# Optimization experiments

Measured on AMD Instinct MI355X. Metric: run time of the kernel, lower is better.

## Reference

```python
import jax, jax.numpy as jnp
import numpy as np

E, S, V_OBS, OBJ, H, L, V_COMM = 64, 64, 128, 16, 256, 32, 32
K = 2 * OBJ  # expected number of nonzero indices per step


def prelu(x, a):
    return jnp.where(x >= 0, x, a * x)


def setup_inputs() -> dict:
    key = jax.random.key(0)
    ks = jax.random.split(key, 32)
    # obs: multi-hot with exactly K ones per (episode, step)
    u = jax.random.uniform(ks[0], (E, S, V_OBS))
    idx = jnp.argsort(u, axis=-1)[..., :K]
    obs = jax.nn.one_hot(idx, V_OBS, dtype=jnp.float32).sum(-2)
    comm = jax.random.normal(ks[1], (E, S, L, V_COMM), jnp.float32)

    def w(k, shape):
        return (jax.random.normal(k, shape, jnp.float32) * 0.05)

    a = lambda: jnp.asarray(0.25, jnp.float32)  # PReLU init
    b = lambda n: jnp.full((n,), 0.01, jnp.float32)
    return dict(
        obs=obs, comm=comm,
        obs_emb=w(ks[2], (V_OBS, H)), obs_a_emb=a(),
        obs_W=w(ks[3], (K * H, H)), obs_b=b(H), obs_a=a(),
        comm_emb=w(ks[4], (V_COMM, H)), comm_a_emb=a(),
        cw1=w(ks[5], (H // 4, H, 1)), cb1=b(H // 4),
        cw3=w(ks[6], (H // 4, H, 3)), cb3=b(H // 4),
        cw5=w(ks[7], (H // 4, H, 5)), cb5=b(H // 4),
        cw7=w(ks[8], (H // 4, H, 7)), cb7=b(H // 4),
        bn_g=jnp.ones((H,), jnp.float32), bn_b=jnp.zeros((H,), jnp.float32), cnn_a=a(),
        Wx=w(ks[9], (3, H, H)), bx=jnp.full((3, H), 0.01, jnp.float32),
        Wh=w(ks[10], (3, H, H)), bh=jnp.full((3, H), 0.01, jnp.float32),
        lin_a1=a(), lin_W=w(ks[11], (H, H)), lin_b=b(H), lin_a2=a(),
    )


def reference(obs, comm, obs_emb, obs_a_emb, obs_W, obs_b, obs_a,
              comm_emb, comm_a_emb, cw1, cb1, cw3, cb3, cw5, cb5, cw7, cb7,
              bn_g, bn_b, cnn_a, Wx, bx, Wh, bh, lin_a1, lin_W, lin_b, lin_a2):
    Ep, St, _ = obs.shape
    # extract_and_concatenate: ascending indices of the K ones per (episode, step)
    idx = jnp.argsort(-obs, axis=-1)[..., :K]          # stable sort -> ascending nonzero idx
    oe = prelu(obs_emb[idx], obs_a_emb)                # [E,S,K,H]
    o = prelu(oe.reshape(Ep, St, K * H) @ obs_W + obs_b, obs_a)  # [E,S,H]

    # comm path (comm already at max_comm_len, pad_zeros is identity)
    tok = jnp.argmax(comm, axis=-1)                    # [E,S,L]
    ce = prelu(comm_emb[tok], comm_a_emb)              # [E,S,L,H]
    x = ce.reshape(Ep * St, L, H).transpose(0, 2, 1)   # [N,H,L]
    dn = ('NCH', 'OIH', 'NCH')
    conv = lambda w_, b_: jax.lax.conv_general_dilated(
        x, w_, (1,), 'SAME', dimension_numbers=dn) + b_[None, :, None]
    y = jnp.concatenate([conv(cw1, cb1), conv(cw3, cb3),
                         conv(cw5, cb5), conv(cw7, cb7)], axis=1)  # [N,H,L]
    # BatchNorm1d (training-mode batch statistics over N and L)
    m = y.mean(axis=(0, 2), keepdims=True)
    v = y.var(axis=(0, 2), keepdims=True)
    y = bn_g[None, :, None] * (y - m) / jnp.sqrt(v + 1e-5) + bn_b[None, :, None]
    y = prelu(y, cnn_a).transpose(0, 2, 1)             # [N,L,H]

    # MTRNN (time_constant=True -> new=1, old=0): GRU-like gated cell
    xproj = jnp.einsum('nlh,ghk->glnk', y, Wx) + bx[:, None, None, :]  # [3,L,N,H]
    h0 = jnp.zeros((Ep * St, H), y.dtype)

    def step(h, xs):
        xr, xz, xn = xs
        r = jax.nn.sigmoid(xr + h @ Wh[0] + bh[0])
        z = jax.nn.sigmoid(xz + h @ Wh[1] + bh[1])
        n = jnp.tanh(xn + r * (h @ Wh[2] + bh[2]))
        return n * (1 - z) + h * z, None

    hN, _ = jax.lax.scan(step, h0, (xproj[0], xproj[1], xproj[2]))  # last step == outputs[:,-1]
    c = hN.reshape(Ep, St, H)
    c = prelu(prelu(c, lin_a1) @ lin_W + lin_b, lin_a2)
    return jnp.concatenate([o, c], axis=-1)           # [E,S,2H]
```

## Files before the change

### kernel.cpp

```cpp
#include <hip/hip_runtime.h>
#include <hip/hip_bf16.h>

#define N_ 4096
#define VOBS 128
#define KOBS 32
#define H_ 256
#define L_ 32
#define VCOMM 32

typedef __attribute__((ext_vector_type(8))) short short8;
typedef __attribute__((ext_vector_type(4))) float floatx4;

__device__ __forceinline__ float prelu_f(float x, float a){ return x >= 0.f ? x : a*x; }
__device__ __forceinline__ ushort f2bf(float x){
  unsigned int u = __float_as_uint(x);
  u = (u + 0x7FFFu + ((u >> 16) & 1u)) >> 16;
  return (ushort)u;
}
__device__ __forceinline__ float bf2f(ushort x){
  unsigned int u = ((unsigned int)x) << 16;
  return __uint_as_float(u);
}

__device__ __forceinline__ void gl_lds16(const ushort* __restrict__ src, ushort* dst){
  __builtin_amdgcn_global_load_lds(
      (const __attribute__((address_space(1))) unsigned int*)src,
      (__attribute__((address_space(3))) unsigned int*)dst, 16, 0, 0);
}


__global__ __launch_bounds__(256) void k_idx(const float* __restrict__ obs, int* __restrict__ idx){
  const int n = blockIdx.x*4 + (threadIdx.x >> 6);
  const int lane = threadIdx.x & 63;
  float v0 = obs[(size_t)n*VOBS + lane];
  float v1 = obs[(size_t)n*VOBS + 64 + lane];
  unsigned long long m0 = __ballot(v0 > 0.5f);
  unsigned long long m1 = __ballot(v1 > 0.5f);
  unsigned long long lt = (1ull << lane) - 1ull;
  if (v0 > 0.5f){
    int pos = __popcll(m0 & lt);
    if (pos < KOBS) idx[n*KOBS + pos] = lane;
  }
  if (v1 > 0.5f){
    int pos = __popcll(m0) + __popcll(m1 & lt);
    if (pos < KOBS) idx[n*KOBS + pos] = 64 + lane;
  }
}

__global__ __launch_bounds__(256) void k_contrib(
    const float* __restrict__ obs_emb, const float* __restrict__ a_emb_p,
    const float* __restrict__ obs_W, float* __restrict__ contrib){
  const int k = blockIdx.x;
  const int vbase = blockIdx.y*16;
  const int tid = threadIdx.x;
  __shared__ float pe[16][H_];
  float a = a_emb_p[0];
  for (int i = tid; i < 16*H_; i += 256){
    int v = i >> 8, j = i & 255;
    pe[v][j] = prelu_f(obs_emb[(size_t)(vbase+v)*H_ + j], a);
  }
  __syncthreads();
  float acc[16];
  #pragma unroll
  for (int v = 0; v < 16; ++v) acc[v] = 0.f;
  for (int j = 0; j < H_; ++j){
    float w = obs_W[((size_t)(k*H_ + j))*H_ + tid];
    #pragma unroll
    for (int v = 0; v < 16; ++v) acc[v] += pe[v][j]*w;
  }
  for (int v = 0; v < 16; ++v)
    contrib[((size_t)((vbase+v)*KOBS + k))*H_ + tid] = acc[v];
}

__global__ __launch_bounds__(256) void k_obs_o(
    const int* __restrict__ idx, const float* __restrict__ contrib,
    const float* __restrict__ obs_b, const float* __restrict__ obs_a_p,
    float* __restrict__ out){
  const int n = blockIdx.x, tid = threadIdx.x;
  __shared__ int id[KOBS];
  if (tid < KOBS) id[tid] = idx[n*KOBS + tid];
  __syncthreads();
  float acc = obs_b[tid];
  #pragma unroll 8
  for (int k = 0; k < KOBS; ++k)
    acc += contrib[((size_t)(id[k]*KOBS + k))*H_ + tid];
  out[(size_t)n*512 + tid] = prelu_f(acc, obs_a_p[0]);
}


__global__ void k_tok(const float* __restrict__ comm, int* __restrict__ tok){
  int i = blockIdx.x*blockDim.x + threadIdx.x;
  if (i >= N_*L_) return;
  const float4* p = (const float4*)(comm + (size_t)i*VCOMM);
  float best = -1e30f; int bi = 0;
  #pragma unroll
  for (int j = 0; j < 8; ++j){
    float4 q = p[j];
    if (q.x > best){ best = q.x; bi = j*4+0; }
    if (q.y > best){ best = q.y; bi = j*4+1; }
    if (q.z > best){ best = q.z; bi = j*4+2; }
    if (q.w > best){ best = q.w; bi = j*4+3; }
  }
  tok[i] = bi;
}

__global__ void k_P(const float* __restrict__ comm_emb, const float* __restrict__ ca_p,
                    const float* __restrict__ cw1, const float* __restrict__ cw3,
                    const float* __restrict__ cw5, const float* __restrict__ cw7,
                    float* __restrict__ P){
  const int slot = blockIdx.x, v = blockIdx.y, c = threadIdx.x;
  int g, tap;
  if (slot == 0){ g=0; tap=0; }
  else if (slot < 4){ g=1; tap=slot-1; }
  else if (slot < 9){ g=2; tap=slot-4; }
  else { g=3; tap=slot-9; }
  const float* w; int ks;
  if (g==0){ w=cw1; ks=1; } else if (g==1){ w=cw3; ks=3; }
  else if (g==2){ w=cw5; ks=5; } else { w=cw7; ks=7; }
  float a = ca_p[0];
  float acc = 0.f;
  for (int h = 0; h < H_; ++h){
    float e = prelu_f(comm_emb[(size_t)v*H_ + h], a);
    acc += e * w[(size_t)(c*H_ + h)*ks + tap];
  }
  P[(size_t)(slot*VCOMM + v)*64 + c] = acc;
}

template<int KS, bool APPLY>
__device__ __forceinline__ void conv_work(
    const float* __restrict__ Ps, const int tk[16][L_], int wave, int lane,
    float bias, float scale, float shift, float ca,
    ushort* __restrict__ ynorm, int nbase, int g,
    float* s_out, float* q_out)
{
  constexpr int PAD = (KS-1)/2;
  float s = 0.f, sq = 0.f;
  for (int j = 0; j < 4; ++j){
    const int nn = wave*4 + j;
    int base[L_];
    #pragma unroll
    for (int l = 0; l < L_; ++l) base[l] = tk[nn][l]*64 + lane;
    #pragma unroll
    for (int l = 0; l < L_; ++l){
      float acc = bias;
      #pragma unroll
      for (int t = 0; t < KS; ++t){
        const int lp = l + t - PAD;
        if (lp >= 0 && lp < L_) acc += Ps[t*2048 + base[lp]];
      }
      if (APPLY){
        float y = prelu_f(fmaf(acc, scale, shift), ca);
        ynorm[((size_t)l*N_ + (nbase+nn))*H_ + g*64 + lane] = f2bf(y);
      } else {
        s += acc; sq += acc*acc;
      }
    }
  }
  *s_out = s; *q_out = sq;
}

__global__ __launch_bounds__(256) void k_conv_stats(
    const int* __restrict__ tok, const float* __restrict__ P,
    const float* __restrict__ cb1, const float* __restrict__ cb3,
    const float* __restrict__ cb5, const float* __restrict__ cb7,
    float* __restrict__ stats){
  const int g = blockIdx.y;
  const int nbase = blockIdx.x*16;
  const int tid = threadIdx.x, lane = tid & 63, wave = tid >> 6;
  const int ks = 2*g + 1, base = g*g;
  const float* cb = (g==0)?cb1:(g==1)?cb3:(g==2)?cb5:cb7;
  const float bias = cb[lane];
  __shared__ float Ps[7*2048];
  __shared__ int tk[16][L_];
  __shared__ float red_s[4][64], red_q[4][64];
  for (int i = tid; i < ks*512; i += 256)
    ((float4*)Ps)[i] = ((const float4*)(P + base*2048))[i];
  for (int i = tid; i < 16*L_; i += 256)
    tk[i>>5][i&31] = tok[(size_t)(nbase + (i>>5))*L_ + (i&31)];
  __syncthreads();
  float s = 0.f, sq = 0.f;
  switch (g){
    case 0: conv_work<1,false>(Ps, tk, wave, lane, bias, 0,0,0, nullptr, nbase, g, &s, &sq); break;
    case 1: conv_work<3,false>(Ps, tk, wave, lane, bias, 0,0,0, nullptr, nbase, g, &s, &sq); break;
    case 2: conv_work<5,false>(Ps, tk, wave, lane, bias, 0,0,0, nullptr, nbase, g, &s, &sq); break;
    default: conv_work<7,false>(Ps, tk, wave, lane, bias, 0,0,0, nullptr, nbase, g, &s, &sq); break;
  }
  red_s[wave][lane] = s; red_q[wave][lane] = sq;
  __syncthreads();
  if (wave == 0){
    float ts = red_s[0][lane]+red_s[1][lane]+red_s[2][lane]+red_s[3][lane];
    float tq = red_q[0][lane]+red_q[1][lane]+red_q[2][lane]+red_q[3][lane];
    atomicAdd(&stats[g*64 + lane], ts);
    atomicAdd(&stats[256 + g*64 + lane], tq);
  }
}

__global__ void k_bn_fin(const float* __restrict__ stats, const float* __restrict__ bn_g,
                         const float* __restrict__ bn_b, float* __restrict__ ss){
  int t = threadIdx.x;
  const float cnt = (float)(N_*L_);
  float m = stats[t]/cnt;
  float v = stats[256+t]/cnt - m*m;
  float sc = bn_g[t] / sqrtf(v + 1e-5f);
  ss[t] = sc; ss[256+t] = bn_b[t] - m*sc;
}

__global__ __launch_bounds__(256) void k_conv_apply(
    const int* __restrict__ tok, const float* __restrict__ P,
    const float* __restrict__ cb1, const float* __restrict__ cb3,
    const float* __restrict__ cb5, const float* __restrict__ cb7,
    const float* __restrict__ ss, const float* __restrict__ cnn_a_p,
    ushort* __restrict__ ynorm){
  const int g = blockIdx.y;
  const int nbase = blockIdx.x*16;
  const int tid = threadIdx.x, lane = tid & 63, wave = tid >> 6;
  const int ks = 2*g + 1, base = g*g;
  const float* cb = (g==0)?cb1:(g==1)?cb3:(g==2)?cb5:cb7;
  const float bias = cb[lane];
  const float scale = ss[g*64 + lane], shift = ss[256 + g*64 + lane];
  const float ca = cnn_a_p[0];
  __shared__ float Ps[7*2048];
  __shared__ int tk[16][L_];
  for (int i = tid; i < ks*512; i += 256)
    ((float4*)Ps)[i] = ((const float4*)(P + base*2048))[i];
  for (int i = tid; i < 16*L_; i += 256)
    tk[i>>5][i&31] = tok[(size_t)(nbase + (i>>5))*L_ + (i&31)];
  __syncthreads();
  float s, q;
  switch (g){
    case 0: conv_work<1,true>(Ps, tk, wave, lane, bias, scale, shift, ca, ynorm, nbase, g, &s, &q); break;
    case 1: conv_work<3,true>(Ps, tk, wave, lane, bias, scale, shift, ca, ynorm, nbase, g, &s, &q); break;
    case 2: conv_work<5,true>(Ps, tk, wave, lane, bias, scale, shift, ca, ynorm, nbase, g, &s, &q); break;
    default: conv_work<7,true>(Ps, tk, wave, lane, bias, scale, shift, ca, ynorm, nbase, g, &s, &q); break;
  }
}


__global__ void k_WT3(const float* __restrict__ Wx, const float* __restrict__ Wh,
                      ushort* __restrict__ WxT3, ushort* __restrict__ WhT3g){
  int id = blockIdx.x*256 + threadIdx.x;
  int g = id >> 16, u = (id >> 8) & 255, k = id & 255;
  float vx = Wx[(size_t)g*65536 + k*256 + u];
  float vh = Wh[(size_t)g*65536 + k*256 + u];
  WxT3[id] = f2bf(vx);
  int w = u >> 5, t = (u >> 4) & 1, l16 = u & 15;
  int row = w*96 + g*32 + t*16 + l16;
  WhT3g[(size_t)row*256 + k] = f2bf(vh);
}

__global__ __launch_bounds__(256,2) void k_xproj(
    const ushort* __restrict__ Y, const ushort* __restrict__ WxT3,
    ushort* __restrict__ xp)
{
  extern __shared__ __align__(16) char smem[];
  ushort* Bs = (ushort*)smem;
  ushort* Tb = (ushort*)smem + 33792;
  const int bm = blockIdx.x;
  const int tid = threadIdx.x, lane = tid & 63, w = tid >> 6;
  const int wm = w >> 1, wn = w & 1;
  const int quad = lane >> 4, l16 = lane & 15;

  short8 Af[4][8];
  #pragma unroll
  for (int mi = 0; mi < 4; ++mi)
    #pragma unroll
    for (int kt = 0; kt < 8; ++kt)
      Af[mi][kt] = *(const short8*)(Y + ((size_t)(bm*128 + wm*64 + mi*16 + l16))*H_ + kt*32 + quad*8);

  for (int bn = 0; bn < 6; ++bn){
    __syncthreads();
    #pragma unroll
    for (int i = 0; i < 16; ++i){
      int id = i*256 + tid;
      int row = id >> 5, cc = id & 31;
      *(uint4*)&Bs[row*264 + cc*8] = *(const uint4*)(WxT3 + ((size_t)(bn*128 + row))*H_ + cc*8);
    }
    __syncthreads();
    floatx4 acc[4][4];
    #pragma unroll
    for (int i = 0; i < 4; ++i)
      #pragma unroll
      for (int j = 0; j < 4; ++j)
        acc[i][j] = (floatx4){0.f,0.f,0.f,0.f};
    #pragma unroll
    for (int kt = 0; kt < 8; ++kt){
      short8 b[4];
      #pragma unroll
      for (int ni = 0; ni < 4; ++ni)
        b[ni] = *(const short8*)&Bs[(wn*64 + ni*16 + l16)*264 + kt*32 + quad*8];
      #pragma unroll
      for (int mi = 0; mi < 4; ++mi)
        #pragma unroll
        for (int ni = 0; ni < 4; ++ni)
          acc[mi][ni] = __builtin_amdgcn_mfma_f32_16x16x32_bf16(Af[mi][kt], b[ni], acc[mi][ni], 0,0,0);
    }
    ushort* Tw = Tb + w*16*72;
    #pragma unroll
    for (int mi = 0; mi < 4; ++mi){
      #pragma unroll
      for (int ni = 0; ni < 4; ++ni)
        #pragma unroll
        for (int r = 0; r < 4; ++r)
          Tw[(quad*4 + r)*72 + ni*16 + l16] = f2bf(acc[mi][ni][r]);
      #pragma unroll
      for (int i = 0; i < 2; ++i){
        int rr = i*8 + (lane >> 3);
        int cc = lane & 7;
        int grow = bm*128 + wm*64 + mi*16 + rr;
        *(uint4*)(xp + (size_t)grow*768 + bn*128 + wn*64 + cc*8) = *(const uint4*)&Tw[rr*72 + cc*8];
      }
    }
  }
}

__global__ __launch_bounds__(512) void k_scan(
    const ushort* __restrict__ Whg, const ushort* __restrict__ xp,
    const float* __restrict__ bx, const float* __restrict__ bh,
    const float* __restrict__ h_in, const ushort* __restrict__ hbf_in,
    float* __restrict__ h_out, ushort* __restrict__ hbf_out, int first)
{
  extern __shared__ __align__(16) char smem[];
  ushort* hA = (ushort*)smem;
  ushort* xs = (ushort*)(smem + 8448);

  const int tid = threadIdx.x;
  const int lane = tid & 63, w = tid >> 6;
  const int quad = lane >> 4, l16 = lane & 15;
  const int n0 = blockIdx.x*16;
  const int u0 = w*32;
  const ushort* Wbase = Whg + (size_t)(w*96)*256;

  float hreg[2][4];
  if (first){
    #pragma unroll
    for (int t = 0; t < 2; ++t)
      #pragma unroll
      for (int r = 0; r < 4; ++r) hreg[t][r] = 0.f;
    for (int i = tid; i < 16*264; i += 512) hA[i] = 0;
  } else {
    #pragma unroll
    for (int t = 0; t < 2; ++t)
      #pragma unroll
      for (int r = 0; r < 4; ++r){
        int row = quad*4 + r, u = u0 + t*16 + l16;
        hreg[t][r] = h_in[(size_t)(n0+row)*H_ + u];
        hA[row*264 + u] = hbf_in[(size_t)(n0+row)*H_ + u];
      }
  }
  float c0[2], c1[2], c2x[2], c2h[2];
  #pragma unroll
  for (int t = 0; t < 2; ++t){
    int u = u0 + t*16 + l16;
    c0[t] = bx[u] + bh[u];
    c1[t] = bx[256+u] + bh[256+u];
    c2x[t] = bx[512+u]; c2h[t] = bh[512+u];
  }

  {
    const ushort* src = xp + (size_t)n0*768;
    #pragma unroll
    for (int t = 0; t < 3; ++t){
      int off = (w*3 + t)*512;
      gl_lds16(src + off + lane*8, xs + off);
    }
  }
  __syncthreads();

  for (int l = 0; l < 16; ++l){
    if (l < 15){
      const ushort* src = xp + (size_t)(l+1)*N_*768 + (size_t)n0*768;
      ushort* dst = xs + ((l+1)&1)*12288;
      #pragma unroll
      for (int t = 0; t < 3; ++t){
        int off = (w*3 + t)*512;
        gl_lds16(src + off + lane*8, dst + off);
      }
    }
    floatx4 acc[3][2];
    #pragma unroll
    for (int g = 0; g < 3; ++g)
      #pragma unroll
      for (int t = 0; t < 2; ++t)
        acc[g][t] = (floatx4){0.f,0.f,0.f,0.f};
    #pragma unroll
    for (int kt = 0; kt < 8; ++kt){
      short8 a = *(const short8*)&hA[l16*264 + kt*32 + quad*8];
      #pragma unroll
      for (int g = 0; g < 3; ++g)
        #pragma unroll
        for (int t = 0; t < 2; ++t){
          short8 b = *(const short8*)(Wbase + (size_t)(g*32 + t*16 + l16)*256 + kt*32 + quad*8);
          acc[g][t] = __builtin_amdgcn_mfma_f32_16x16x32_bf16(a, b, acc[g][t], 0,0,0);
        }
    }
    __syncthreads();
    const ushort* xc = xs + (l&1)*12288;
    #pragma unroll
    for (int t = 0; t < 2; ++t){
      const int u = u0 + t*16 + l16;
      #pragma unroll
      for (int r = 0; r < 4; ++r){
        const int row = quad*4 + r;
        float xr = bf2f(xc[row*768 +       u]);
        float xz = bf2f(xc[row*768 + 256 + u]);
        float xn = bf2f(xc[row*768 + 512 + u]);
        float rg = 1.f/(1.f + __expf(-(xr + acc[0][t][r] + c0[t])));
        float zg = 1.f/(1.f + __expf(-(xz + acc[1][t][r] + c1[t])));
        float na = xn + c2x[t] + rg*(acc[2][t][r] + c2h[t]);
        float ng = 1.f - 2.f/(1.f + __expf(2.f*na));
        hreg[t][r] = ng*(1.f - zg) + hreg[t][r]*zg;
        hA[row*264 + u] = f2bf(hreg[t][r]);
      }
    }
    __syncthreads();
  }
  #pragma unroll
  for (int t = 0; t < 2; ++t)
    #pragma unroll
    for (int r = 0; r < 4; ++r){
      int row = quad*4 + r, u = u0 + t*16 + l16;
      h_out[(size_t)(n0+row)*H_ + u] = hreg[t][r];
      hbf_out[(size_t)(n0+row)*H_ + u] = f2bf(hreg[t][r]);
    }
}

__global__ __launch_bounds__(256) void k_final(
    const float* __restrict__ h, const float* __restrict__ a1p,
    const float* __restrict__ lin_W, const float* __restrict__ lin_b,
    const float* __restrict__ a2p, float* __restrict__ out){
  const int nbase = blockIdx.x*16, tid = threadIdx.x;
  __shared__ float hp[16][H_];
  const float a1 = a1p[0], a2 = a2p[0];
  for (int i = tid; i < 16*H_; i += 256)
    hp[i>>8][i&255] = prelu_f(h[(size_t)(nbase + (i>>8))*H_ + (i&255)], a1);
  __syncthreads();
  float acc[16];
  const float b = lin_b[tid];
  #pragma unroll
  for (int r = 0; r < 16; ++r) acc[r] = b;
  for (int j = 0; j < H_; ++j){
    float w = lin_W[(size_t)j*H_ + tid];
    #pragma unroll
    for (int r = 0; r < 16; ++r) acc[r] += hp[r][j]*w;
  }
  for (int r = 0; r < 16; ++r)
    out[(size_t)(nbase+r)*512 + 256 + tid] = prelu_f(acc[r], a2);
}

extern "C" void kernel_launch(void* const* d_in, const int* in_sizes, int n_in,
                              void* d_out, int out_size, void* d_ws, size_t ws_size,
                              hipStream_t stream) {
  (void)in_sizes; (void)n_in; (void)out_size; (void)ws_size;
  const float* obs      = (const float*)d_in[0];
  const float* comm     = (const float*)d_in[1];
  const float* obs_emb  = (const float*)d_in[2];
  const float* obs_a_emb= (const float*)d_in[3];
  const float* obs_W    = (const float*)d_in[4];
  const float* obs_b    = (const float*)d_in[5];
  const float* obs_a    = (const float*)d_in[6];
  const float* comm_emb = (const float*)d_in[7];
  const float* comm_a   = (const float*)d_in[8];
  const float* cw1      = (const float*)d_in[9];
  const float* cb1      = (const float*)d_in[10];
  const float* cw3      = (const float*)d_in[11];
  const float* cb3      = (const float*)d_in[12];
  const float* cw5      = (const float*)d_in[13];
  const float* cb5      = (const float*)d_in[14];
  const float* cw7      = (const float*)d_in[15];
  const float* cb7      = (const float*)d_in[16];
  const float* bn_g     = (const float*)d_in[17];
  const float* bn_b     = (const float*)d_in[18];
  const float* cnn_a    = (const float*)d_in[19];
  const float* Wx       = (const float*)d_in[20];
  const float* bx       = (const float*)d_in[21];
  const float* Wh       = (const float*)d_in[22];
  const float* bh       = (const float*)d_in[23];
  const float* lin_a1   = (const float*)d_in[24];
  const float* lin_W    = (const float*)d_in[25];
  const float* lin_b    = (const float*)d_in[26];
  const float* lin_a2   = (const float*)d_in[27];
  float* out = (float*)d_out;

  char* ws = (char*)d_ws;
  float*  contrib = (float*)(ws + 0);
  float*  P       = (float*)(ws + 4194304);
  int*    idx     = (int*)  (ws + 4325376);
  int*    tok     = (int*)  (ws + 4849664);
  float*  stats   = (float*)(ws + 5373952);
  float*  ss      = (float*)(ws + 5376000);
  ushort* WxT3    = (ushort*)(ws + 5378048);
  ushort* WhT3g   = (ushort*)(ws + 5771264);
  float*  h_a     = (float*)(ws + 6164480);
  float*  h_b     = (float*)(ws + 10358784);
  ushort* hbf_a   = (ushort*)(ws + 14553088);
  ushort* hbf_b   = (ushort*)(ws + 16650240);
  ushort* ynorm   = (ushort*)(ws + 18747392);
  ushort* xp      = (ushort*)(ws + 85856256);

  hipMemsetAsync(stats, 0, 512*sizeof(float), stream);

  k_idx<<<1024, 256, 0, stream>>>(obs, idx);
  k_tok<<<512, 256, 0, stream>>>(comm, tok);
  k_WT3<<<768, 256, 0, stream>>>(Wx, Wh, WxT3, WhT3g);
  k_P<<<dim3(16,32), 64, 0, stream>>>(comm_emb, comm_a, cw1, cw3, cw5, cw7, P);
  k_contrib<<<dim3(32,8), 256, 0, stream>>>(obs_emb, obs_a_emb, obs_W, contrib);
  k_obs_o<<<4096, 256, 0, stream>>>(idx, contrib, obs_b, obs_a, out);
  k_conv_stats<<<dim3(256,4), 256, 0, stream>>>(tok, P, cb1, cb3, cb5, cb7, stats);
  k_bn_fin<<<1, 256, 0, stream>>>(stats, bn_g, bn_b, ss);
  k_conv_apply<<<dim3(256,4), 256, 0, stream>>>(tok, P, cb1, cb3, cb5, cb7, ss, cnn_a, ynorm);

  k_xproj<<<512, 256, 76800, stream>>>(ynorm, WxT3, xp);
  k_scan<<<256, 512, 57600, stream>>>(WhT3g, xp, bx, bh, h_a, hbf_a, h_a, hbf_a, 1);
  k_xproj<<<512, 256, 76800, stream>>>(ynorm + (size_t)16*N_*H_, WxT3, xp);
  k_scan<<<256, 512, 57600, stream>>>(WhT3g, xp, bx, bh, h_a, hbf_a, h_b, hbf_b, 0);

  k_final<<<256, 256, 0, stream>>>(h_b, lin_a1, lin_W, lin_b, lin_a2, out);
}
```

Measured before the change: 574.5 us.

## Retile xproj GEMM into a 2D grid with K-sliced LDS tiles; partially unroll scan

The input-projection GEMM previously held a 128-row A tile in registers and looped over six N tiles per block with a large dynamic LDS buffer. It now launches a 512x6 grid in which each block stages 32-wide K slices of both A and B in small static LDS tiles. That cuts register and LDS pressure, raises occupancy and parallelism, and removes the serial N loop, at the cost of reloading the A rows once per N tile and syncing at every K step. The scan kernel's inner K loop is also reduced to unroll 2, trading instruction-level parallelism for lower register pressure.

```diff
diff --git a/kernel.cpp b/kernel.cpp
--- a/kernel.cpp
+++ b/kernel.cpp
@@ -248,67 +248,65 @@
   WhT3g[(size_t)row*256 + k] = f2bf(vh);
 }
 
-__global__ __launch_bounds__(256,2) void k_xproj(
+__global__ __launch_bounds__(256) void k_xproj(
     const ushort* __restrict__ Y, const ushort* __restrict__ WxT3,
     ushort* __restrict__ xp)
 {
-  extern __shared__ __align__(16) char smem[];
-  ushort* Bs = (ushort*)smem;
-  ushort* Tb = (ushort*)smem + 33792;
-  const int bm = blockIdx.x;
+  __shared__ __align__(16) ushort As[128][40];
+  __shared__ __align__(16) ushort Bs[128][40];
+  __shared__ __align__(16) ushort Tb[4][16][72];
+  const int bm = blockIdx.x, bn = blockIdx.y;
   const int tid = threadIdx.x, lane = tid & 63, w = tid >> 6;
   const int wm = w >> 1, wn = w & 1;
   const int quad = lane >> 4, l16 = lane & 15;
 
-  short8 Af[4][8];
-  #pragma unroll
-  for (int mi = 0; mi < 4; ++mi)
-    #pragma unroll
-    for (int kt = 0; kt < 8; ++kt)
-      Af[mi][kt] = *(const short8*)(Y + ((size_t)(bm*128 + wm*64 + mi*16 + l16))*H_ + kt*32 + quad*8);
-
-  for (int bn = 0; bn < 6; ++bn){
+  floatx4 acc[4][4];
+  #pragma unroll
+  for (int i = 0; i < 4; ++i)
+    #pragma unroll
+    for (int j = 0; j < 4; ++j)
+      acc[i][j] = (floatx4){0.f,0.f,0.f,0.f};
+
+  const ushort* Abase = Y + (size_t)bm*128*H_;
+  const ushort* Bbase = WxT3 + (size_t)bn*128*H_;
+
+  for (int kt = 0; kt < 8; ++kt){
     __syncthreads();
     #pragma unroll
-    for (int i = 0; i < 16; ++i){
-      int id = i*256 + tid;
-      int row = id >> 5, cc = id & 31;
-      *(uint4*)&Bs[row*264 + cc*8] = *(const uint4*)(WxT3 + ((size_t)(bn*128 + row))*H_ + cc*8);
+    for (int i = 0; i < 2; ++i){
+      int chunk = i*256 + tid;
+      int row = chunk >> 2, kc = chunk & 3;
+      *(uint4*)&As[row][kc*8] = *(const uint4*)(Abase + (size_t)row*H_ + kt*32 + kc*8);
+      *(uint4*)&Bs[row][kc*8] = *(const uint4*)(Bbase + (size_t)row*H_ + kt*32 + kc*8);
     }
     __syncthreads();
-    floatx4 acc[4][4];
-    #pragma unroll
-    for (int i = 0; i < 4; ++i)
-      #pragma unroll
-      for (int j = 0; j < 4; ++j)
-        acc[i][j] = (floatx4){0.f,0.f,0.f,0.f};
-    #pragma unroll
-    for (int kt = 0; kt < 8; ++kt){
-      short8 b[4];
+    short8 a[4], b[4];
+    #pragma unroll
+    for (int mi = 0; mi < 4; ++mi)
+      a[mi] = *(const short8*)&As[wm*64 + mi*16 + l16][quad*8];
+    #pragma unroll
+    for (int ni = 0; ni < 4; ++ni)
+      b[ni] = *(const short8*)&Bs[wn*64 + ni*16 + l16][quad*8];
+    #pragma unroll
+    for (int mi = 0; mi < 4; ++mi)
       #pragma unroll
       for (int ni = 0; ni < 4; ++ni)
-        b[ni] = *(const short8*)&Bs[(wn*64 + ni*16 + l16)*264 + kt*32 + quad*8];
-      #pragma unroll
-      for (int mi = 0; mi < 4; ++mi)
-        #pragma unroll
-        for (int ni = 0; ni < 4; ++ni)
-          acc[mi][ni] = __builtin_amdgcn_mfma_f32_16x16x32_bf16(Af[mi][kt], b[ni], acc[mi][ni], 0,0,0);
-    }
-    ushort* Tw = Tb + w*16*72;
-    #pragma unroll
-    for (int mi = 0; mi < 4; ++mi){
-      #pragma unroll
-      for (int ni = 0; ni < 4; ++ni)
-        #pragma unroll
-        for (int r = 0; r < 4; ++r)
-          Tw[(quad*4 + r)*72 + ni*16 + l16] = f2bf(acc[mi][ni][r]);
-      #pragma unroll
-      for (int i = 0; i < 2; ++i){
-        int rr = i*8 + (lane >> 3);
-        int cc = lane & 7;
-        int grow = bm*128 + wm*64 + mi*16 + rr;
-        *(uint4*)(xp + (size_t)grow*768 + bn*128 + wn*64 + cc*8) = *(const uint4*)&Tw[rr*72 + cc*8];
-      }
+        acc[mi][ni] = __builtin_amdgcn_mfma_f32_16x16x32_bf16(a[mi], b[ni], acc[mi][ni], 0,0,0);
+  }
+  ushort* Tw = &Tb[w][0][0];
+  #pragma unroll
+  for (int mi = 0; mi < 4; ++mi){
+    #pragma unroll
+    for (int ni = 0; ni < 4; ++ni)
+      #pragma unroll
+      for (int r = 0; r < 4; ++r)
+        Tw[(quad*4 + r)*72 + ni*16 + l16] = f2bf(acc[mi][ni][r]);
+    #pragma unroll
+    for (int i = 0; i < 2; ++i){
+      int rr = i*8 + (lane >> 3);
+      int cc = lane & 7;
+      int grow = bm*128 + wm*64 + mi*16 + rr;
+      *(uint4*)(xp + (size_t)grow*768 + bn*128 + wn*64 + cc*8) = *(const uint4*)&Tw[rr*72 + cc*8];
     }
   }
 }
@@ -382,7 +380,7 @@
       #pragma unroll
       for (int t = 0; t < 2; ++t)
         acc[g][t] = (floatx4){0.f,0.f,0.f,0.f};
-    #pragma unroll
+    #pragma unroll 2
     for (int kt = 0; kt < 8; ++kt){
       short8 a = *(const short8*)&hA[l16*264 + kt*32 + quad*8];
       #pragma unroll
@@ -509,9 +507,9 @@
   k_bn_fin<<<1, 256, 0, stream>>>(stats, bn_g, bn_b, ss);
   k_conv_apply<<<dim3(256,4), 256, 0, stream>>>(tok, P, cb1, cb3, cb5, cb7, ss, cnn_a, ynorm);
 
-  k_xproj<<<512, 256, 76800, stream>>>(ynorm, WxT3, xp);
+  k_xproj<<<dim3(512,6), 256, 0, stream>>>(ynorm, WxT3, xp);
   k_scan<<<256, 512, 57600, stream>>>(WhT3g, xp, bx, bh, h_a, hbf_a, h_a, hbf_a, 1);
-  k_xproj<<<512, 256, 76800, stream>>>(ynorm + (size_t)16*N_*H_, WxT3, xp);
+  k_xproj<<<dim3(512,6), 256, 0, stream>>>(ynorm + (size_t)16*N_*H_, WxT3, xp);
   k_scan<<<256, 512, 57600, stream>>>(WhT3g, xp, bx, bh, h_a, hbf_a, h_b, hbf_b, 0);
 
   k_final<<<256, 256, 0, stream>>>(h_b, lin_a1, lin_W, lin_b, lin_a2, out);
```

Result: slower. 812.4 us (+41.4%).
